# Kernel tuning notes

Measured on AMD Instinct MI355X. Metric: run time of the kernel, lower is better.

Reference implementation:

```python
import jax, jax.numpy as jnp
import numpy as np
from math import factorial

N_NODES = 100000
N_EDGES = 1600000
HIDDEN = 8
N_GRAPHS = 64
RC = 1.5            # PolynomialCutoff radius
CUT_P = 6           # polynomial cutoff exponent (DimeNet-style)
GB_SIGMA = 0.1      # GaussianBasisExpansion width
GB_NUM = 10
GB_LO, GB_HI = 0.7, 1.7
LN2 = 0.6931471805599453

def _cgc(j1, m1, j2, m2, j3, m3):
    if m1 + m2 != m3:
        return 0.0
    f = factorial
    pre = ((2*j3+1) * f(j3+j1-j2) * f(j3-j1+j2) * f(j1+j2-j3) / f(j1+j2+j3+1)) ** 0.5
    pre *= (f(j3+m3)*f(j3-m3)*f(j1-m1)*f(j1+m1)*f(j2-m2)*f(j2+m2)) ** 0.5
    s = 0.0
    for k in range(max(0, j2-j3-m1, j1-j3+m2), min(j1+j2-j3, j1-m1, j2+m2) + 1):
        s += (-1)**k / (f(k)*f(j1+j2-j3-k)*f(j1-m1-k)*f(j2+m2-k)*f(j3-j2+m1+k)*f(j3-j1-m2+k))
    return pre * s

def _u(l):
    # complex -> real spherical-harmonic change of basis; rows indexed by real m = -l..l
    U = np.zeros((2*l+1, 2*l+1), dtype=complex)
    U[l, l] = 1.0
    for m in range(1, l+1):
        U[l+m, l+m] = (-1)**m / np.sqrt(2.0)
        U[l+m, l-m] = 1.0 / np.sqrt(2.0)
        U[l-m, l-m] = 1j / np.sqrt(2.0)
        U[l-m, l+m] = -1j * (-1)**m / np.sqrt(2.0)
    return U

def _real_cg(l1, l2, l3):
    cgc = np.zeros((2*l1+1, 2*l2+1, 2*l3+1), dtype=complex)
    for m1 in range(-l1, l1+1):
        for m2 in range(-l2, l2+1):
            m3 = m1 + m2
            if -l3 <= m3 <= l3:
                cgc[l1+m1, l2+m2, l3+m3] = _cgc(l1, m1, l2, m2, l3, m3)
    W = np.einsum('ai,bj,ck,ijk->cab', _u(l1), _u(l2), np.conj(_u(l3)), cgc)
    re, im = np.real(W), np.imag(W)
    w = re if np.abs(re).sum() >= np.abs(im).sum() else im
    return jnp.asarray(w, dtype=jnp.float32)  # (2l3+1, 2l1+1, 2l2+1)

_TRIPLES = [(0,0,0),(0,1,1),(1,0,1),(1,1,0),(1,1,1),(1,2,1)]
CG = {t: _real_cg(*t) for t in _TRIPLES}
PATHS1 = [(0,0,0),(0,1,1)]                                    # L_in=0, L_edge=2, L_out=1
PATHS2 = [(0,0,0),(0,1,1),(1,0,1),(1,1,0),(1,1,1),(1,2,1)]    # L_in=1, L_edge=2, L_out=1
PATHS3 = [(0,0,0),(1,1,0)]                                    # L_in=1, L_edge=2, L_out=0
DEG_L1 = jnp.array([0, 1, 1, 1])  # degree of each order slot for L = 0..1
DEG_L0 = jnp.array([0])

def _ssp(x):
    return jax.nn.softplus(x) - LN2

def _so3_linear(x, sh, w, paths, n_out_orders, channel_wise):
    # x: (E, in_orders, Cin); sh: (E, edge_orders); w: (E,P,C) or (E,P,Cin,Cout)
    E = x.shape[0]
    c_out = w.shape[-1]
    out = jnp.zeros((E, n_out_orders, c_out), x.dtype)
    for p, (l1, l2, l3) in enumerate(paths):
        cg = CG[(l1, l2, l3)]                      # (2l3+1, 2l1+1, 2l2+1)
        xs = x[:, l1*l1:(l1+1)**2, :]
        ss = sh[:, l2*l2:(l2+1)**2]
        m = jnp.einsum('oab,eac,eb->eoc', cg, xs, ss)
        if channel_wise:
            m = m * w[:, p][:, None, :]
        else:
            m = jnp.einsum('eoc,ecd->eod', m, w[:, p])
        out = out.at[:, l3*l3:(l3+1)**2, :].add(m)
    return out

def _norm_act(h, act, degs):
    # NormAct: per-degree, per-channel norm gating x * act(||x||) / ||x||
    parts = []
    for l in degs:
        seg = h[:, l*l:(l+1)**2, :]
        n = jnp.sqrt(jnp.sum(seg*seg, axis=1, keepdims=True) + 1e-12)
        parts.append(seg * (act(n) / n))
    return jnp.concatenate(parts, axis=1)

def _tfn_block(x, src, dst, sh, edge_emb, edge_w, wp_w, wp_b, si_w, paths, n_out_orders, channel_wise, deg_idx):
    E = sh.shape[0]
    c_in = x.shape[-1]
    lw = edge_emb @ wp_w + wp_b                  # weight_producer (per-edge CG path weights)
    P = len(paths)
    if channel_wise:
        lw = lw.reshape(E, P, c_in)
    else:
        lw = lw.reshape(E, P, c_in, -1)
    msg = _so3_linear(x[src], sh, lw, paths, n_out_orders, channel_wise)  # gather + CG TP
    msg = msg * edge_w[:, None, None]
    agg = jax.ops.segment_sum(msg, dst, num_segments=N_NODES)             # scatter-sum
    return jnp.einsum('nmc,mcd->nmd', agg, si_w[deg_idx])                 # DegreeWiseLinear self-interaction

def _forward(x, edge_index, edge_sh, edge_len, batch, wp1_w, wp1_b, wp2_w, wp2_b, wp3_w, wp3_b, si1_w, si2_w, si3_w, out_w, out_b):
    src, dst = edge_index[0], edge_index[1]
    centers = jnp.linspace(GB_LO, GB_HI, GB_NUM)
    edge_emb = jnp.exp(-(edge_len[:, None] - centers[None, :])**2 / (2.0 * GB_SIGMA**2))
    u = edge_len / RC
    p = CUT_P
    cut = 1.0 - (p+1)*(p+2)/2.0*u**p + p*(p+2)*u**(p+1) - p*(p+1)/2.0*u**(p+2)
    edge_w = jnp.where(u < 1.0, cut, 0.0)
    h = x[:, None, :]                                   # (N, 1 order, 1 channel)
    h = _tfn_block(h, src, dst, edge_sh, edge_emb, edge_w, wp1_w, wp1_b, si1_w, PATHS1, 4, False, DEG_L1)
    h = _norm_act(h, _ssp, (0, 1))
    h = _tfn_block(h, src, dst, edge_sh, edge_emb, edge_w, wp2_w, wp2_b, si2_w, PATHS2, 4, True, DEG_L1)
    h = _norm_act(h, _ssp, (0, 1))
    h = _tfn_block(h, src, dst, edge_sh, edge_emb, edge_w, wp3_w, wp3_b, si3_w, PATHS3, 1, True, DEG_L0)
    h = jax.nn.silu(h)
    g = jax.ops.segment_sum(h[:, 0, :], batch, num_segments=N_GRAPHS)   # SumAggregation pool
    return jax.nn.softmax(g @ out_w + out_b, axis=-1)

def setup_inputs():
    key = jax.random.key(0)
    ks = jax.random.split(key, 16)
    H = HIDDEN
    s = lambda k, shp: jax.random.normal(k, shp, jnp.float32) * 0.1
    return {
        'x': jax.random.normal(ks[0], (N_NODES, 1), jnp.float32),
        'edge_index': jax.random.randint(ks[1], (2, N_EDGES), 0, N_NODES),
        'edge_sh': jax.random.normal(ks[2], (N_EDGES, 9), jnp.float32),
        'edge_len': jax.random.uniform(ks[3], (N_EDGES,), jnp.float32) * 1.5,
        'batch': jnp.sort(jax.random.randint(ks[4], (N_NODES,), 0, N_GRAPHS)),
        'wp1_w': s(ks[5], (10, 2*H)), 'wp1_b': jnp.zeros((2*H,), jnp.float32),
        'wp2_w': s(ks[6], (10, 6*H)), 'wp2_b': jnp.zeros((6*H,), jnp.float32),
        'wp3_w': s(ks[7], (10, 2*H)), 'wp3_b': jnp.zeros((2*H,), jnp.float32),
        'si1_w': s(ks[8], (2, H, H)), 'si2_w': s(ks[9], (2, H, H)), 'si3_w': s(ks[10], (1, H, H)),
        'out_w': s(ks[11], (H, 8)), 'out_b': jnp.zeros((8,), jnp.float32),
    }

def reference(x, edge_index, edge_sh, edge_len, batch, wp1_w, wp1_b, wp2_w, wp2_b, wp3_w, wp3_b, si1_w, si2_w, si3_w, out_w, out_b):
    return _forward(x, edge_index, edge_sh, edge_len, batch, wp1_w, wp1_b, wp2_w, wp2_b, wp3_w, wp3_b, si1_w, si2_w, si3_w, out_w, out_b)
```

## Files before the change

kernel.cpp:

```cpp
#include <hip/hip_runtime.h>
#include <hip/hip_fp16.h>
#include <math.h>
#include <complex>

#define NN 100000
#define NE 1600000
#define NG 64
#define NBUCK 782
#define SCB 256
#define SEB 6250
#define TBINS 256
#define TB2   128
#define MAXB  2560
#define NBLK_E   6250
#define NBLK_N8  3125
#define NBLK_SCAN 391

struct CGTables {
  float c000;
  float c011[3][3];
  float c101[3][3];
  float c110[3][3];
  float c111[3][3][3];
  float c121[3][3][5];
};
struct CGConsts {
  float c000;
  float l011, l101, l110, l111;
  float s121[5][5];
};

static double hfact(int n){ double r=1.0; for(int i=2;i<=n;++i) r*=(double)i; return r; }

static double host_cgc(int j1,int m1,int j2,int m2,int j3,int m3){
  if (m1+m2 != m3) return 0.0;
  double pre = sqrt((2.0*j3+1.0)*hfact(j3+j1-j2)*hfact(j3-j1+j2)*hfact(j1+j2-j3)/hfact(j1+j2+j3+1));
  pre *= sqrt(hfact(j3+m3)*hfact(j3-m3)*hfact(j1-m1)*hfact(j1+m1)*hfact(j2-m2)*hfact(j2+m2));
  int k0 = 0; if (j2-j3-m1 > k0) k0 = j2-j3-m1; if (j1-j3+m2 > k0) k0 = j1-j3+m2;
  int k1 = j1+j2-j3; if (j1-m1 < k1) k1 = j1-m1; if (j2+m2 < k1) k1 = j2+m2;
  double s = 0.0;
  for (int k=k0;k<=k1;++k){
    double t = 1.0/(hfact(k)*hfact(j1+j2-j3-k)*hfact(j1-m1-k)*hfact(j2+m2-k)*hfact(j3-j2+m1+k)*hfact(j3-j1-m2+k));
    s += (k&1) ? -t : t;
  }
  return pre*s;
}

typedef std::complex<double> cd;

static void host_u(int l, cd U[5][5]){
  for (int a=0;a<5;++a) for (int b=0;b<5;++b) U[a][b] = 0.0;
  U[l][l] = 1.0;
  const double is2 = 1.0/sqrt(2.0);
  for (int m=1;m<=l;++m){
    double sgn = (m&1) ? -1.0 : 1.0;
    U[l+m][l+m] = sgn*is2;
    U[l+m][l-m] = is2;
    U[l-m][l-m] = cd(0.0, is2);
    U[l-m][l+m] = cd(0.0, -sgn*is2);
  }
}

static void host_real_cg(int l1,int l2,int l3, float* out){
  cd U1[5][5], U2[5][5], U3[5][5];
  host_u(l1,U1); host_u(l2,U2); host_u(l3,U3);
  int n1=2*l1+1, n2=2*l2+1, n3=2*l3+1;
  double cgt[5][5][5];
  for (int i=0;i<5;++i) for (int j=0;j<5;++j) for (int k=0;k<5;++k) cgt[i][j][k]=0.0;
  for (int m1=-l1;m1<=l1;++m1) for (int m2=-l2;m2<=l2;++m2){
    int m3 = m1+m2;
    if (m3 >= -l3 && m3 <= l3) cgt[l1+m1][l2+m2][l3+m3] = host_cgc(l1,m1,l2,m2,l3,m3);
  }
  cd W[5][5][5];
  double sre=0.0, sim=0.0;
  for (int c=0;c<n3;++c) for (int a=0;a<n1;++a) for (int b=0;b<n2;++b){
    cd acc = 0.0;
    for (int i=0;i<n1;++i) for (int j=0;j<n2;++j) for (int k=0;k<n3;++k)
      acc += U1[a][i]*U2[b][j]*std::conj(U3[c][k])*cgt[i][j][k];
    W[c][a][b] = acc;
    sre += fabs(acc.real()); sim += fabs(acc.imag());
  }
  bool use_re = (sre >= sim);
  for (int c=0;c<n3;++c) for (int a=0;a<n1;++a) for (int b=0;b<n2;++b)
    out[(c*n1+a)*n2+b] = (float)(use_re ? W[c][a][b].real() : W[c][a][b].imag());
}

static void build_cg_tables(CGTables& t){
  float w000[1];  host_real_cg(0,0,0,w000); t.c000 = w000[0];
  float w011[9];  host_real_cg(0,1,1,w011);
  for (int o=0;o<3;++o) for (int b=0;b<3;++b) t.c011[o][b] = w011[o*3+b];
  float w101[9];  host_real_cg(1,0,1,w101);
  for (int o=0;o<3;++o) for (int a=0;a<3;++a) t.c101[o][a] = w101[o*3+a];
  float w110[9];  host_real_cg(1,1,0,w110);
  for (int a=0;a<3;++a) for (int b=0;b<3;++b) t.c110[a][b] = w110[a*3+b];
  float w111[27]; host_real_cg(1,1,1,w111);
  for (int o=0;o<3;++o) for (int a=0;a<3;++a) for (int b=0;b<3;++b) t.c111[o][a][b] = w111[(o*3+a)*3+b];
  float w121[45]; host_real_cg(1,2,1,w121);
  for (int o=0;o<3;++o) for (int a=0;a<3;++a) for (int b=0;b<5;++b) t.c121[o][a][b] = w121[(o*3+a)*5+b];
}

static void build_cg_consts(const CGTables& t, CGConsts& K){
  K.c000 = t.c000;
  K.l011 = t.c011[0][0];
  K.l101 = t.c101[0][0];
  K.l110 = t.c110[0][0];
  K.l111 = t.c111[0][1][2];
  const int pi[5] = {0,0,0,1,1};
  const int pj[5] = {0,1,2,1,2};
  for (int p=0;p<5;++p)
    for (int b=0;b<5;++b)
      K.s121[p][b] = 0.5f*(t.c121[pi[p]][pj[p]][b] + t.c121[pj[p]][pi[p]][b]);
}

__device__ __forceinline__ float sspf(float v){
  float sp = (v > 30.0f) ? v : log1pf(expf(v));
  return sp - 0.69314718055994531f;
}

__device__ __forceinline__ float cutoff_w(float len){
  float u = len * (1.0f/1.5f);
  float u2 = u*u, u6 = u2*u2*u2, u7 = u6*u, u8 = u7*u;
  float cut = 1.0f - 28.0f*u6 + 48.0f*u7 - 21.0f*u8;
  return (u < 1.0f) ? cut : 0.0f;
}

__device__ __forceinline__ float pack2h(float a, float b){
  __half2 h = __floats2half2_rn(a, b);
  return *reinterpret_cast<float*>(&h);
}
__device__ __forceinline__ float2 unpack2h(float f){
  __half2 h = *reinterpret_cast<__half2*>(&f);
  return __half22float2(h);
}

__global__ __launch_bounds__(256) void lwtab_kernel(
    const float* __restrict__ wpw, const float* __restrict__ wpb,
    int NP, int bins, float* __restrict__ tab)
{
  int idx = blockIdx.x*256 + threadIdx.x;
  int tot = bins*NP*8;
  if (idx >= tot) return;
  int stride = NP*8;
  int bin = idx / stride;
  int r = idx - bin*stride;
  float len = (1.5f/(bins-1)) * bin;
  float v = wpb[r];
  #pragma unroll
  for (int i=0;i<10;++i){
    float dd = len - (0.7f + (float)i*(1.0f/9.0f));
    v = fmaf(wpw[i*stride + r], __expf(-50.0f*dd*dd), v);
  }
  tab[idx] = v;
}

__global__ __launch_bounds__(1024) void bhist_kernel(const int* __restrict__ dst, int* __restrict__ bcnt){
  __shared__ int cnt[NBUCK];
  for (int j=threadIdx.x; j<NBUCK; j+=1024) cnt[j] = 0;
  __syncthreads();
  int base = blockIdx.x * SEB;
  for (int i=threadIdx.x; i<SEB; i+=1024)
    atomicAdd(&cnt[dst[base+i] >> 7], 1);
  __syncthreads();
  for (int j=threadIdx.x; j<NBUCK; j+=1024)
    if (cnt[j]) atomicAdd(&bcnt[j], cnt[j]);
}

__global__ __launch_bounds__(1024) void bscan_kernel(const int* __restrict__ bcnt,
                                                     int* __restrict__ bbase, int* __restrict__ bclaim){
  __shared__ int s[1024];
  int t = threadIdx.x;
  int v = (t < NBUCK) ? bcnt[t] : 0;
  s[t] = v; __syncthreads();
  for (int off=1; off<1024; off<<=1){
    int u = (t >= off) ? s[t-off] : 0;
    __syncthreads();
    s[t] += u;
    __syncthreads();
  }
  if (t < NBUCK){
    int excl = s[t] - v;
    bbase[t] = excl;
    bclaim[t] = excl;
    if (t == NBUCK-1) bbase[NBUCK] = excl + v;
  }
}

__global__ __launch_bounds__(1024) void scatter_rec_kernel(
    const int* __restrict__ src, const int* __restrict__ dst,
    const float* __restrict__ sh, const float* __restrict__ elen,
    const float* __restrict__ x,
    int* __restrict__ bclaim, float4* __restrict__ rec, CGConsts K)
{
  __shared__ int cnt[NBUCK];
  __shared__ int bs[NBUCK];
  for (int j=threadIdx.x; j<NBUCK; j+=1024) cnt[j] = 0;
  __syncthreads();
  int base = blockIdx.x * SEB;
  for (int i=threadIdx.x; i<SEB; i+=1024)
    atomicAdd(&cnt[dst[base+i] >> 7], 1);
  __syncthreads();
  for (int j=threadIdx.x; j<NBUCK; j+=1024){
    int c = cnt[j];
    if (c) bs[j] = atomicAdd(&bclaim[j], c);
    cnt[j] = 0;
  }
  __syncthreads();
  for (int i=threadIdx.x; i<SEB; i+=1024){
    int e = base + i;
    int d = dst[e];
    int b = d >> 7;
    int off = atomicAdd(&cnt[b], 1);
    int slot = bs[b] + off;
    float len = elen[e];
    float w = cutoff_w(len);
    const float* shr = sh + (size_t)e*9;
    float sh0 = shr[0]*w, shx = shr[1]*w, shy = shr[2]*w, shz = shr[3]*w;
    float b0 = shr[4], b1 = shr[5], b2 = shr[6], b3 = shr[7], b4 = shr[8];
    float S[5];
    #pragma unroll
    for (int p=0;p<5;++p)
      S[p] = (K.s121[p][0]*b0 + K.s121[p][1]*b1 + K.s121[p][2]*b2 + K.s121[p][3]*b3 + K.s121[p][4]*b4)*w;
    int sn = src[e];
    float x0 = x[sn];
    int packed = sn | ((d & 127) << 20);
    float4* rp = rec + (size_t)slot*2;
    rp[0] = make_float4(__int_as_float(packed), len, pack2h(sh0, shx), pack2h(shy, shz));
    rp[1] = make_float4(pack2h(S[0], S[1]), pack2h(S[2], S[3]), S[4], x0);
  }
}

__global__ __launch_bounds__(512) void sortcopy_kernel(
    const float4* __restrict__ recin, const int* __restrict__ bbase,
    float4* __restrict__ recout, int* __restrict__ rowptr)
{
  __shared__ int hist[128], offs[128], cur[128];
  __shared__ short outmap[MAXB];
  int b = blockIdx.x;
  int e0 = bbase[b], e1 = bbase[b+1];
  int cnt = e1 - e0;
  int t = threadIdx.x;
  if (t < 128) hist[t] = 0;
  __syncthreads();
  for (int i=t; i<cnt; i+=512){
    int packed = __float_as_int(recin[(size_t)(e0+i)*2].x);
    atomicAdd(&hist[packed >> 20], 1);
  }
  __syncthreads();
  if (t < 128) offs[t] = hist[t];
  __syncthreads();
  for (int off=1; off<128; off<<=1){
    int v = (t < 128 && t >= off) ? offs[t-off] : 0;
    __syncthreads();
    if (t < 128) offs[t] += v;
    __syncthreads();
  }
  int n0 = b << 7;
  int nn = NN - n0; if (nn > 128) nn = 128;
  if (t < 128){
    int excl = offs[t] - hist[t];
    cur[t] = excl;
    if (t < nn) rowptr[n0+t] = e0 + excl;
  }
  if (b == NBUCK-1 && t == 0) rowptr[NN] = NE;
  __syncthreads();
  for (int i=t; i<cnt; i+=512){
    int packed = __float_as_int(recin[(size_t)(e0+i)*2].x);
    int r = atomicAdd(&cur[packed >> 20], 1);
    outmap[r] = (short)i;
  }
  __syncthreads();
  for (int o=t; o<cnt; o+=512){
    int j = outmap[o];
    const float4* rin = recin + (size_t)(e0+j)*2;
    float4* rout = recout + (size_t)(e0+o)*2;
    float4 a = rin[0], bq = rin[1];
    rout[0] = a; rout[1] = bq;
  }
}

__global__ __launch_bounds__(256) void deg_hist_kernel(const int* __restrict__ rowptr, int* __restrict__ dcnt){
  __shared__ int lb[256];
  lb[threadIdx.x] = 0; __syncthreads();
  int n = blockIdx.x*256 + threadIdx.x;
  if (n < NN){
    int d = rowptr[n+1]-rowptr[n]; if (d > 255) d = 255;
    atomicAdd(&lb[d], 1);
  }
  __syncthreads();
  if (lb[threadIdx.x]) atomicAdd(&dcnt[threadIdx.x], lb[threadIdx.x]);
}

__global__ void deg_scan_kernel(const int* __restrict__ dcnt, int* __restrict__ dcur){
  __shared__ int s[256];
  int t = threadIdx.x;
  int v = dcnt[t];
  s[t] = v; __syncthreads();
  for (int off=1; off<256; off<<=1){
    int u = (t >= off) ? s[t-off] : 0;
    __syncthreads();
    s[t] += u;
    __syncthreads();
  }
  dcur[t] = s[t] - v;
}

__global__ __launch_bounds__(256) void deg_scatter_kernel(const int* __restrict__ rowptr,
                                                          int* __restrict__ dcur, int* __restrict__ perm){
  __shared__ int lcnt[256];
  __shared__ int lbase[256];
  int t = threadIdx.x;
  lcnt[t] = 0;
  __syncthreads();
  int n = blockIdx.x*256 + t;
  int d = 0, lrank = 0;
  bool valid = (n < NN);
  if (valid){
    d = rowptr[n+1]-rowptr[n]; if (d > 255) d = 255;
    lrank = atomicAdd(&lcnt[d], 1);
  }
  __syncthreads();
  int cnt = lcnt[t];
  if (cnt > 0) lbase[t] = atomicAdd(&dcur[t], cnt);
  __syncthreads();
  if (valid) perm[lbase[d] + lrank] = n;
}

__global__ __launch_bounds__(256) void gather1_kernel(
    const int* __restrict__ rowptr, const int* __restrict__ perm,
    const float4* __restrict__ rec, const float* __restrict__ tab,
    const float* __restrict__ si, float* __restrict__ out, CGConsts K)
{
  __shared__ float lwt[TBINS*16];
  for (int i=threadIdx.x; i<TBINS*16; i+=256) lwt[i] = tab[i];
  __syncthreads();
  int gid = blockIdx.x*256 + threadIdx.x;
  int c = gid & 7;
  int n = perm[gid >> 3];
  int r0 = rowptr[n], r1 = rowptr[n+1];
  float a0=0.f, a1=0.f, a2=0.f, a3=0.f;
  #pragma unroll 2
  for (int s=r0; s<r1; ++s){
    const float4* rp = rec + (size_t)s*2;
    float4 q0 = rp[0];
    float4 q1 = rp[1];
    float len = q0.y;
    float2 s01 = unpack2h(q0.z);
    float2 s23 = unpack2h(q0.w);
    float sh0 = s01.x, shx = s01.y, shy = s23.x, shz = s23.y;
    float x0 = q1.w;
    float fb = len * ((TBINS-1)/1.5f);
    int bin = (int)fb; if (bin > TBINS-2) bin = TBINS-2;
    float fr = fb - (float)bin;
    int tb = bin*16 + c;
    float lw0 = fmaf(fr, lwt[tb+16]-lwt[tb], lwt[tb]);
    float lw1 = fmaf(fr, lwt[tb+24]-lwt[tb+8], lwt[tb+8]);
    a0 = fmaf(K.c000*sh0, x0*lw0, a0);
    float t = K.l011*x0*lw1;
    a1 = fmaf(t, shx, a1); a2 = fmaf(t, shy, a2); a3 = fmaf(t, shz, a3);
  }
  float z0=0.f, z1=0.f, z2=0.f, z3=0.f;
  #pragma unroll
  for (int k=0;k<8;++k){
    float y0 = __shfl(a0,k,8), y1 = __shfl(a1,k,8), y2 = __shfl(a2,k,8), y3 = __shfl(a3,k,8);
    float w0 = si[k*8+c], w1 = si[64+k*8+c];
    z0 = fmaf(y0,w0,z0); z1 = fmaf(y1,w1,z1); z2 = fmaf(y2,w1,z2); z3 = fmaf(y3,w1,z3);
  }
  float n0 = sqrtf(z0*z0 + 1e-12f);
  float r0v = z0*(sspf(n0)/n0);
  float nv = sqrtf(z1*z1 + z2*z2 + z3*z3 + 1e-12f);
  float sc = sspf(nv)/nv;
  float4 o = make_float4(r0v, z1*sc, z2*sc, z3*sc);
  *reinterpret_cast<float4*>(out + ((size_t)n*8 + c)*4) = o;
}

__global__ __launch_bounds__(256) void gather2_kernel(
    const float* __restrict__ hin,
    const int* __restrict__ rowptr, const int* __restrict__ perm,
    const float4* __restrict__ rec, const float* __restrict__ tab,
    const float* __restrict__ si, float* __restrict__ out, CGConsts K)
{
  __shared__ float lwt[TB2*48];
  for (int i=threadIdx.x; i<TB2*48; i+=256) lwt[i] = tab[i];
  __syncthreads();
  int gid = blockIdx.x*256 + threadIdx.x;
  int c = gid & 7;
  int n = perm[gid >> 3];
  int r0 = rowptr[n], r1 = rowptr[n+1];
  float a0=0.f, a1=0.f, a2=0.f, a3=0.f;
  #pragma unroll 2
  for (int s=r0; s<r1; ++s){
    const float4* rp = rec + (size_t)s*2;
    float4 q0 = rp[0];
    float4 q1 = rp[1];
    int sn = __float_as_int(q0.x) & 0xFFFFF;
    float len = q0.y;
    float2 s01 = unpack2h(q0.z);
    float2 s23 = unpack2h(q0.w);
    float sh0 = s01.x, shx = s01.y, shy = s23.x, shz = s23.y;
    float2 Sa = unpack2h(q1.x);
    float2 Sb = unpack2h(q1.y);
    float S00 = Sa.x, S01 = Sa.y, S02 = Sb.x, S11 = Sb.y, S12 = q1.z;
    float S22 = -S00 - S11;
    float4 hv = *reinterpret_cast<const float4*>(hin + ((size_t)sn*8 + c)*4);
    float x0 = hv.x, xa0 = hv.y, xa1 = hv.z, xa2 = hv.w;
    float fb = len * ((TB2-1)/1.5f);
    int bin = (int)fb; if (bin > TB2-2) bin = TB2-2;
    float fr = fb - (float)bin;
    int tb = bin*48 + c;
    float lw[6];
    #pragma unroll
    for (int p=0;p<6;++p){
      float t0v = lwt[tb + p*8];
      float t1v = lwt[tb + 48 + p*8];
      lw[p] = fmaf(fr, t1v - t0v, t0v);
    }
    float shdotx = shx*xa0 + shy*xa1 + shz*xa2;
    a0 += K.c000*sh0*x0*lw[0] + K.l110*shdotx*lw[3];
    float t011 = K.l011*x0*lw[1];
    float t101 = K.l101*sh0*lw[2];
    float l4 = K.l111*lw[4];
    float sx0 = S00*xa0 + S01*xa1 + S02*xa2;
    float sx1 = S01*xa0 + S11*xa1 + S12*xa2;
    float sx2 = S02*xa0 + S12*xa1 + S22*xa2;
    a1 += t011*shx + t101*xa0 + l4*(xa1*shz - xa2*shy) + sx0*lw[5];
    a2 += t011*shy + t101*xa1 + l4*(xa2*shx - xa0*shz) + sx1*lw[5];
    a3 += t011*shz + t101*xa2 + l4*(xa0*shy - xa1*shx) + sx2*lw[5];
  }
  float z0=0.f, z1=0.f, z2=0.f, z3=0.f;
  #pragma unroll
  for (int k=0;k<8;++k){
    float y0 = __shfl(a0,k,8), y1 = __shfl(a1,k,8), y2 = __shfl(a2,k,8), y3 = __shfl(a3,k,8);
    float w0 = si[k*8+c], w1 = si[64+k*8+c];
    z0 = fmaf(y0,w0,z0); z1 = fmaf(y1,w1,z1); z2 = fmaf(y2,w1,z2); z3 = fmaf(y3,w1,z3);
  }
  float n0 = sqrtf(z0*z0 + 1e-12f);
  float r0v = z0*(sspf(n0)/n0);
  float nv = sqrtf(z1*z1 + z2*z2 + z3*z3 + 1e-12f);
  float sc = sspf(nv)/nv;
  float4 o = make_float4(r0v, z1*sc, z2*sc, z3*sc);
  *reinterpret_cast<float4*>(out + ((size_t)n*8 + c)*4) = o;
}

__global__ __launch_bounds__(256) void gather3_kernel(
    const float* __restrict__ hin, const int* __restrict__ rowptr, const int* __restrict__ perm,
    const float4* __restrict__ rec, const float* __restrict__ tab,
    const float* __restrict__ si, const int* __restrict__ batch,
    float* __restrict__ G, CGConsts K)
{
  __shared__ float lwt[TBINS*16];
  __shared__ float lg[512];
  for (int i=threadIdx.x; i<TBINS*16; i+=256) lwt[i] = tab[i];
  lg[threadIdx.x] = 0.f; lg[256+threadIdx.x] = 0.f;
  __syncthreads();
  int gid = blockIdx.x*256 + threadIdx.x;
  int c = gid & 7;
  int n = perm[gid >> 3];
  int r0 = rowptr[n], r1 = rowptr[n+1];
  float acc = 0.f;
  #pragma unroll 2
  for (int s=r0; s<r1; ++s){
    float4 q0 = rec[(size_t)s*2];
    int sn = __float_as_int(q0.x) & 0xFFFFF;
    float len = q0.y;
    float2 s01 = unpack2h(q0.z);
    float2 s23 = unpack2h(q0.w);
    float sh0 = s01.x, shx = s01.y, shy = s23.x, shz = s23.y;
    float4 hv = *reinterpret_cast<const float4*>(hin + ((size_t)sn*8 + c)*4);
    float fb = len * ((TBINS-1)/1.5f);
    int bin = (int)fb; if (bin > TBINS-2) bin = TBINS-2;
    float fr = fb - (float)bin;
    int tb = bin*16 + c;
    float lw0 = fmaf(fr, lwt[tb+16]-lwt[tb], lwt[tb]);
    float lw1 = fmaf(fr, lwt[tb+24]-lwt[tb+8], lwt[tb+8]);
    float shdotx = shx*hv.y + shy*hv.z + shz*hv.w;
    acc += K.c000*sh0*hv.x*lw0 + K.l110*shdotx*lw1;
  }
  float z = 0.f;
  #pragma unroll
  for (int k=0;k<8;++k){
    float y = __shfl(acc,k,8);
    z = fmaf(y, si[k*8+c], z);
  }
  float v = z / (1.0f + expf(-z));
  atomicAdd(&lg[batch[n]*8 + c], v);
  __syncthreads();
  int t = threadIdx.x;
  float v0 = lg[t];     if (v0 != 0.f) unsafeAtomicAdd(&G[t], v0);
  float v1 = lg[256+t]; if (v1 != 0.f) unsafeAtomicAdd(&G[256+t], v1);
}

__global__ void final_kernel(
    const float* __restrict__ g, const float* __restrict__ ow,
    const float* __restrict__ ob, float* __restrict__ out)
{
  int i = threadIdx.x;
  if (i >= NG) return;
  float gv[8];
  #pragma unroll
  for (int c=0;c<8;++c) gv[c] = g[i*8+c];
  float lg[8];
  #pragma unroll
  for (int j=0;j<8;++j){
    float acc = ob[j];
    #pragma unroll
    for (int c=0;c<8;++c) acc += gv[c]*ow[c*8+j];
    lg[j] = acc;
  }
  float mx = lg[0];
  #pragma unroll
  for (int j=1;j<8;++j) mx = fmaxf(mx, lg[j]);
  float ssum = 0.0f;
  #pragma unroll
  for (int j=0;j<8;++j){ lg[j] = expf(lg[j]-mx); ssum += lg[j]; }
  float inv = 1.0f/ssum;
  #pragma unroll
  for (int j=0;j<8;++j) out[i*8+j] = lg[j]*inv;
}

__global__ __launch_bounds__(256) void edge1_kernel(
    const float* __restrict__ x, const int* __restrict__ src, const int* __restrict__ dst,
    const float* __restrict__ sh, const float* __restrict__ elen,
    const float* __restrict__ wpw, const float* __restrict__ wpb,
    float* __restrict__ agg, CGTables cg)
{
  __shared__ float sw[176];
  for (int i=threadIdx.x;i<176;i+=256) sw[i] = (i<160) ? wpw[i] : wpb[i-160];
  __syncthreads();
  int e = blockIdx.x*256 + threadIdx.x;
  if (e >= NE) return;
  float len = elen[e];
  float lw[16];
  #pragma unroll
  for (int j=0;j<16;++j) lw[j] = sw[160+j];
  #pragma unroll
  for (int i=0;i<10;++i){
    float dd = len - (0.7f + (float)i*(1.0f/9.0f));
    float em = __expf(-50.0f*dd*dd);
    #pragma unroll
    for (int j=0;j<16;++j) lw[j] += em*sw[i*16+j];
  }
  float w = cutoff_w(len);
  int s = src[e], d = dst[e];
  float x0 = x[s];
  const float* shr = sh + (size_t)e*9;
  float sh0 = shr[0], sh1 = shr[1], sh2 = shr[2], sh3 = shr[3];
  float* ag = agg + (size_t)d*32;
  float b0 = cg.c000*x0*sh0*w;
  #pragma unroll
  for (int j=0;j<8;++j) unsafeAtomicAdd(ag+j, b0*lw[j]);
  #pragma unroll
  for (int o=0;o<3;++o){
    float s011 = cg.c011[o][0]*sh1 + cg.c011[o][1]*sh2 + cg.c011[o][2]*sh3;
    float bo = s011*x0*w;
    #pragma unroll
    for (int j=0;j<8;++j) unsafeAtomicAdd(ag+(1+o)*8+j, bo*lw[8+j]);
  }
}

__global__ __launch_bounds__(256) void edge2_kernel(
    const float* __restrict__ h, const int* __restrict__ src, const int* __restrict__ dst,
    const float* __restrict__ sh, const float* __restrict__ elen,
    const float* __restrict__ wpw, const float* __restrict__ wpb,
    float* __restrict__ agg, CGTables cg)
{
  __shared__ float sw[528];
  for (int i=threadIdx.x;i<528;i+=256) sw[i] = (i<480) ? wpw[i] : wpb[i-480];
  __syncthreads();
  int e = blockIdx.x*256 + threadIdx.x;
  if (e >= NE) return;
  float len = elen[e];
  float lw[48];
  #pragma unroll
  for (int j=0;j<48;++j) lw[j] = sw[480+j];
  #pragma unroll
  for (int i=0;i<10;++i){
    float dd = len - (0.7f + (float)i*(1.0f/9.0f));
    float em = __expf(-50.0f*dd*dd);
    #pragma unroll
    for (int j=0;j<48;++j) lw[j] += em*sw[i*48+j];
  }
  float w = cutoff_w(len);
  int s = src[e], d = dst[e];
  float shv[9];
  const float* shr = sh + (size_t)e*9;
  #pragma unroll
  for (int i=0;i<9;++i) shv[i] = shr[i];
  float sh0 = shv[0];
  float s011[3], k110[3], k111[3][3], k121[3][3];
  #pragma unroll
  for (int o=0;o<3;++o) s011[o] = cg.c011[o][0]*shv[1] + cg.c011[o][1]*shv[2] + cg.c011[o][2]*shv[3];
  #pragma unroll
  for (int a=0;a<3;++a) k110[a] = cg.c110[a][0]*shv[1] + cg.c110[a][1]*shv[2] + cg.c110[a][2]*shv[3];
  #pragma unroll
  for (int o=0;o<3;++o)
    #pragma unroll
    for (int a=0;a<3;++a)
      k111[o][a] = cg.c111[o][a][0]*shv[1] + cg.c111[o][a][1]*shv[2] + cg.c111[o][a][2]*shv[3];
  #pragma unroll
  for (int o=0;o<3;++o)
    #pragma unroll
    for (int a=0;a<3;++a){
      float acc = 0.0f;
      #pragma unroll
      for (int b=0;b<5;++b) acc += cg.c121[o][a][b]*shv[4+b];
      k121[o][a] = acc;
    }
  const float4* hr = reinterpret_cast<const float4*>(h + (size_t)s*32);
  float xs[32];
  #pragma unroll
  for (int i=0;i<8;++i){
    float4 q = hr[i];
    xs[i*4] = q.x; xs[i*4+1] = q.y; xs[i*4+2] = q.z; xs[i*4+3] = q.w;
  }
  float* ag = agg + (size_t)d*32;
  #pragma unroll
  for (int c=0;c<8;++c){
    float x0 = xs[c], x1 = xs[8+c], x2 = xs[16+c], x3 = xs[24+c];
    float r0 = cg.c000*sh0*x0*lw[c]
             + (k110[0]*x1 + k110[1]*x2 + k110[2]*x3)*lw[24+c];
    unsafeAtomicAdd(ag+c, r0*w);
    #pragma unroll
    for (int o=0;o<3;++o){
      float r = s011[o]*x0*lw[8+c]
              + (cg.c101[o][0]*x1 + cg.c101[o][1]*x2 + cg.c101[o][2]*x3)*sh0*lw[16+c]
              + (k111[o][0]*x1 + k111[o][1]*x2 + k111[o][2]*x3)*lw[32+c]
              + (k121[o][0]*x1 + k121[o][1]*x2 + k121[o][2]*x3)*lw[40+c];
      unsafeAtomicAdd(ag+(1+o)*8+c, r*w);
    }
  }
}

__global__ __launch_bounds__(256) void edge3_kernel(
    const float* __restrict__ h, const int* __restrict__ src, const int* __restrict__ dst,
    const float* __restrict__ sh, const float* __restrict__ elen,
    const float* __restrict__ wpw, const float* __restrict__ wpb,
    float* __restrict__ agg, CGTables cg)
{
  __shared__ float sw[176];
  for (int i=threadIdx.x;i<176;i+=256) sw[i] = (i<160) ? wpw[i] : wpb[i-160];
  __syncthreads();
  int e = blockIdx.x*256 + threadIdx.x;
  if (e >= NE) return;
  float len = elen[e];
  float lw[16];
  #pragma unroll
  for (int j=0;j<16;++j) lw[j] = sw[160+j];
  #pragma unroll
  for (int i=0;i<10;++i){
    float dd = len - (0.7f + (float)i*(1.0f/9.0f));
    float em = __expf(-50.0f*dd*dd);
    #pragma unroll
    for (int j=0;j<16;++j) lw[j] += em*sw[i*16+j];
  }
  float w = cutoff_w(len);
  int s = src[e], d = dst[e];
  const float* shr = sh + (size_t)e*9;
  float sh0 = shr[0], sh1 = shr[1], sh2 = shr[2], sh3 = shr[3];
  float k110[3];
  #pragma unroll
  for (int a=0;a<3;++a) k110[a] = cg.c110[a][0]*sh1 + cg.c110[a][1]*sh2 + cg.c110[a][2]*sh3;
  const float4* hr = reinterpret_cast<const float4*>(h + (size_t)s*32);
  float xs[32];
  #pragma unroll
  for (int i=0;i<8;++i){
    float4 q = hr[i];
    xs[i*4] = q.x; xs[i*4+1] = q.y; xs[i*4+2] = q.z; xs[i*4+3] = q.w;
  }
  float* ag = agg + (size_t)d*8;
  #pragma unroll
  for (int c=0;c<8;++c){
    float r = cg.c000*sh0*xs[c]*lw[c]
            + (k110[0]*xs[8+c] + k110[1]*xs[16+c] + k110[2]*xs[24+c])*lw[8+c];
    unsafeAtomicAdd(ag+c, r*w);
  }
}

__global__ __launch_bounds__(256) void node_fb_kernel(
    const float* __restrict__ agg, const float* __restrict__ si,
    float* __restrict__ out)
{
  __shared__ float s_si[128];
  if (threadIdx.x < 128) s_si[threadIdx.x] = si[threadIdx.x];
  __syncthreads();
  int idx = blockIdx.x*256 + threadIdx.x;
  if (idx >= NN*8) return;
  int n = idx >> 3, d = idx & 7;
  const float* ar = agg + (size_t)n*32;
  float y[4];
  #pragma unroll
  for (int m=0;m<4;++m){
    const float* sm = s_si + (m ? 64 : 0);
    float acc = 0.0f;
    #pragma unroll
    for (int c=0;c<8;++c) acc += ar[m*8+c]*sm[c*8+d];
    y[m] = acc;
  }
  float n0 = sqrtf(y[0]*y[0] + 1e-12f);
  float r0 = y[0]*(sspf(n0)/n0);
  float n1 = sqrtf(y[1]*y[1] + y[2]*y[2] + y[3]*y[3] + 1e-12f);
  float sc = sspf(n1)/n1;
  float* orow = out + (size_t)n*32;
  orow[d]      = r0;
  orow[8+d]    = y[1]*sc;
  orow[16+d]   = y[2]*sc;
  orow[24+d]   = y[3]*sc;
}

__global__ __launch_bounds__(256) void node3_fb_kernel(
    const float* __restrict__ agg, const float* __restrict__ si,
    const int* __restrict__ batch, float* __restrict__ g)
{
  __shared__ float s_si[64];
  if (threadIdx.x < 64) s_si[threadIdx.x] = si[threadIdx.x];
  __syncthreads();
  int n = blockIdx.x*256 + threadIdx.x;
  if (n >= NN) return;
  const float* ar = agg + (size_t)n*8;
  float av[8];
  #pragma unroll
  for (int c=0;c<8;++c) av[c] = ar[c];
  int b = batch[n];
  float* gr = g + (size_t)b*8;
  #pragma unroll
  for (int d=0;d<8;++d){
    float acc = 0.0f;
    #pragma unroll
    for (int c=0;c<8;++c) acc += av[c]*s_si[c*8+d];
    float v = acc / (1.0f + expf(-acc));
    unsafeAtomicAdd(gr+d, v);
  }
}

extern "C" void kernel_launch(void* const* d_in, const int* in_sizes, int n_in,
                              void* d_out, int out_size, void* d_ws, size_t ws_size,
                              hipStream_t stream)
{
  const float* x     = (const float*)d_in[0];
  const int*   eidx  = (const int*)  d_in[1];
  const float* esh   = (const float*)d_in[2];
  const float* elen  = (const float*)d_in[3];
  const int*   batch = (const int*)  d_in[4];
  const float* wp1w  = (const float*)d_in[5];
  const float* wp1b  = (const float*)d_in[6];
  const float* wp2w  = (const float*)d_in[7];
  const float* wp2b  = (const float*)d_in[8];
  const float* wp3w  = (const float*)d_in[9];
  const float* wp3b  = (const float*)d_in[10];
  const float* si1   = (const float*)d_in[11];
  const float* si2   = (const float*)d_in[12];
  const float* si3   = (const float*)d_in[13];
  const float* outw  = (const float*)d_in[14];
  const float* outb  = (const float*)d_in[15];
  const int* src = eidx;
  const int* dst = eidx + NE;

  CGTables cg;
  build_cg_tables(cg);
  CGConsts K;
  build_cg_consts(cg, K);

  char* p = (char*)d_ws;
  auto carve = [&](size_t bytes) -> void* {
    void* r = (void*)p;
    p += ((bytes + 255)/256)*256;
    return r;
  };
  int*    rowptr = (int*)   carve((NN+1)*4);
  int*    perm   = (int*)   carve(NN*4);
  int*    bcnt   = (int*)   carve((NBUCK+1)*4);
  int*    bbase  = (int*)   carve((NBUCK+1)*4);
  int*    bclaim = (int*)   carve((NBUCK+1)*4);
  int*    dcnt   = (int*)   carve(256*4);
  int*    dcur   = (int*)   carve(256*4);
  float*  tab1   = (float*) carve(TBINS*16*4);
  float*  tab2   = (float*) carve(TB2*48*4);
  float*  tab3   = (float*) carve(TBINS*16*4);
  float*  G      = (float*) carve(512*4);
  float4* bufX   = (float4*)carve((size_t)NE*32);
  float4* bufY   = (float4*)carve((size_t)NE*32);
  size_t need = (size_t)(p - (char*)d_ws);
  float* B1 = (float*)bufX;
  float* B2 = (float*)bufX + (size_t)NN*32;

  if (ws_size >= need){
    hipMemsetAsync(bcnt, 0, (NBUCK+1)*sizeof(int), stream);
    hipMemsetAsync(dcnt, 0, 256*sizeof(int), stream);
    hipMemsetAsync(G, 0, 512*sizeof(float), stream);
    lwtab_kernel<<<(TBINS*16+255)/256, 256, 0, stream>>>(wp1w, wp1b, 2, TBINS, tab1);
    lwtab_kernel<<<(TB2*48+255)/256, 256, 0, stream>>>(wp2w, wp2b, 6, TB2, tab2);
    lwtab_kernel<<<(TBINS*16+255)/256, 256, 0, stream>>>(wp3w, wp3b, 2, TBINS, tab3);
    bhist_kernel<<<SCB, 1024, 0, stream>>>(dst, bcnt);
    bscan_kernel<<<1, 1024, 0, stream>>>(bcnt, bbase, bclaim);
    scatter_rec_kernel<<<SCB, 1024, 0, stream>>>(src, dst, esh, elen, x, bclaim, bufX, K);
    sortcopy_kernel<<<NBUCK, 512, 0, stream>>>(bufX, bbase, bufY, rowptr);
    deg_hist_kernel<<<NBLK_SCAN, 256, 0, stream>>>(rowptr, dcnt);
    deg_scan_kernel<<<1, 256, 0, stream>>>(dcnt, dcur);
    deg_scatter_kernel<<<NBLK_SCAN, 256, 0, stream>>>(rowptr, dcur, perm);
    gather1_kernel<<<NBLK_N8, 256, 0, stream>>>(rowptr, perm, bufY, tab1, si1, B1, K);
    gather2_kernel<<<NBLK_N8, 256, 0, stream>>>(B1, rowptr, perm, bufY, tab2, si2, B2, K);
    gather3_kernel<<<NBLK_N8, 256, 0, stream>>>(B2, rowptr, perm, bufY, tab3, si3, batch, G, K);
    final_kernel<<<1, 64, 0, stream>>>(G, outw, outb, (float*)d_out);
  } else {
    float* A  = (float*)d_ws;
    float* Bf = A + (size_t)NN*32;
    float* Cf = Bf + (size_t)NN*32;
    float* Gf = Cf + (size_t)NN*8;
    hipMemsetAsync(A, 0, (size_t)NN*32*sizeof(float), stream);
    edge1_kernel<<<NBLK_E, 256, 0, stream>>>(x, src, dst, esh, elen, wp1w, wp1b, A, cg);
    node_fb_kernel<<<(NN*8+255)/256, 256, 0, stream>>>(A, si1, Bf);
    hipMemsetAsync(A, 0, (size_t)NN*32*sizeof(float), stream);
    edge2_kernel<<<NBLK_E, 256, 0, stream>>>(Bf, src, dst, esh, elen, wp2w, wp2b, A, cg);
    node_fb_kernel<<<(NN*8+255)/256, 256, 0, stream>>>(A, si2, Bf);
    hipMemsetAsync(Cf, 0, (size_t)NN*8*sizeof(float), stream);
    edge3_kernel<<<NBLK_E, 256, 0, stream>>>(Bf, src, dst, esh, elen, wp3w, wp3b, Cf, cg);
    hipMemsetAsync(Gf, 0, (size_t)NG*8*sizeof(float), stream);
    node3_fb_kernel<<<(NN+255)/256, 256, 0, stream>>>(Cf, si3, batch, Gf);
    final_kernel<<<1, 64, 0, stream>>>(Gf, outw, outb, (float*)d_out);
  }
}
```

Before: 253.0 us.

## Locally sort edges by bucket in shared memory before scattering records

```diff
diff --git a/kernel.cpp b/kernel.cpp
--- a/kernel.cpp
+++ b/kernel.cpp
@@ -193,24 +193,43 @@
 {
   __shared__ int cnt[NBUCK];
   __shared__ int bs[NBUCK];
-  for (int j=threadIdx.x; j<NBUCK; j+=1024) cnt[j] = 0;
+  __shared__ int lstart[NBUCK];
+  __shared__ int s[1024];
+  __shared__ unsigned short lperm[SEB];
+  int t = threadIdx.x;
+  for (int j=t; j<NBUCK; j+=1024) cnt[j] = 0;
   __syncthreads();
   int base = blockIdx.x * SEB;
-  for (int i=threadIdx.x; i<SEB; i+=1024)
+  for (int i=t; i<SEB; i+=1024)
     atomicAdd(&cnt[dst[base+i] >> 7], 1);
   __syncthreads();
-  for (int j=threadIdx.x; j<NBUCK; j+=1024){
+  for (int j=t; j<NBUCK; j+=1024){
     int c = cnt[j];
     if (c) bs[j] = atomicAdd(&bclaim[j], c);
-    cnt[j] = 0;
-  }
-  __syncthreads();
-  for (int i=threadIdx.x; i<SEB; i+=1024){
+  }
+  int v = (t < NBUCK) ? cnt[t] : 0;
+  s[t] = v; __syncthreads();
+  for (int off=1; off<1024; off<<=1){
+    int u = (t >= off) ? s[t-off] : 0;
+    __syncthreads();
+    s[t] += u;
+    __syncthreads();
+  }
+  if (t < NBUCK) lstart[t] = s[t] - v;
+  for (int j=t; j<NBUCK; j+=1024) cnt[j] = 0;
+  __syncthreads();
+  for (int i=t; i<SEB; i+=1024){
+    int b = dst[base+i] >> 7;
+    int off = atomicAdd(&cnt[b], 1);
+    lperm[lstart[b] + off] = (unsigned short)i;
+  }
+  __syncthreads();
+  for (int j=t; j<SEB; j+=1024){
+    int i = lperm[j];
     int e = base + i;
     int d = dst[e];
     int b = d >> 7;
-    int off = atomicAdd(&cnt[b], 1);
-    int slot = bs[b] + off;
+    int slot = bs[b] + (j - lstart[b]);
     float len = elen[e];
     float w = cutoff_w(len);
     const float* shr = sh + (size_t)e*9;
```

Result: slower. 290.0 us (+14.6%).
